# Optimization experiments

Hardware: AMD Instinct MI355X
Metric: run time of the kernel (lower is better)

Reference implementation:

```python
import jax, jax.numpy as jnp
import numpy as np

ALPHA, BETA, GAMMA = 1.0, 0.01, 0.1
COS_EPS = 1e-8  # torch F.cosine_similarity eps


def setup_inputs() -> dict:
    key = jax.random.key(0)
    k1, k2, k3, k4 = jax.random.split(key, 4)
    B, C = 4096, 1000
    N, D = 8192, 256
    return {
        "pred": jax.random.normal(k1, (B, C), dtype=jnp.float32),
        "target": jax.random.randint(k2, (B,), 0, C, dtype=jnp.int64),
        "adj_matrix": jax.random.uniform(k3, (N, N), dtype=jnp.float32),
        "node_embeddings": jax.random.normal(k4, (N, D), dtype=jnp.float32),
    }


def reference(pred, target, adj_matrix, node_embeddings):
    # L_task: mean cross-entropy over logits
    logp = jax.nn.log_softmax(pred, axis=-1)                      # [B, C]
    l_task = -jnp.mean(jnp.take_along_axis(logp, target[:, None], axis=1))

    # L_sparse: mean |adj|
    l_sparse = jnp.mean(jnp.abs(adj_matrix))

    # L_semantic: cosine similarity via normalize + matmul (avoids NxNxD intermediate)
    norms = jnp.linalg.norm(node_embeddings, axis=1)              # [N]
    dots = node_embeddings @ node_embeddings.T                    # [N, N]
    sim = dots / jnp.maximum(norms[:, None] * norms[None, :], COS_EPS)
    l_semantic = jnp.mean(adj_matrix * (1.0 - sim))

    return ALPHA * l_task + BETA * l_sparse + GAMMA * l_semantic
```

## Files before the change

### kernel.cpp

```cpp
#include <hip/hip_runtime.h>
#include <hip/hip_bf16.h>
#include <stdint.h>
#include <stddef.h>

#define N_NODES 8192
#define DIM     256
#define BATCH   4096
#define CLASSES 1000
#define ALPHA_C 1.0f
#define BETA_C  0.01f
#define GAMMA_C 0.1f

typedef __bf16 bf16_t;
typedef __bf16 bf16x8 __attribute__((ext_vector_type(8)));
typedef __bf16 bf16x4 __attribute__((ext_vector_type(4)));
typedef float  f32x4  __attribute__((ext_vector_type(4)));
typedef float  f32x16 __attribute__((ext_vector_type(16)));

__device__ __forceinline__ void async16(const void* g, void* l) {
  __builtin_amdgcn_global_load_lds(
      (const __attribute__((address_space(1))) uint32_t*)g,
      (__attribute__((address_space(3))) uint32_t*)l, 16, 0, 0);
}

__global__ __launch_bounds__(256) void prep_kernel(
    const float* __restrict__ emb, bf16_t* __restrict__ U) {
  const int row = blockIdx.x;
  const int t = threadIdx.x;
  const float v = emb[(size_t)row * DIM + t];
  float sq = v * v;
  for (int off = 32; off; off >>= 1) sq += __shfl_down(sq, off);
  __shared__ float red[4];
  if ((t & 63) == 0) red[t >> 6] = sq;
  __syncthreads();
  const float total = red[0] + red[1] + red[2] + red[3];
  U[(size_t)row * DIM + t] = (bf16_t)(v * rsqrtf(total));
}

__global__ __launch_bounds__(256) void transpose_kernel(
    const bf16_t* __restrict__ U, bf16_t* __restrict__ Ut) {
  __shared__ bf16_t tile[64][72];
  const int i0 = blockIdx.x * 64, d0 = blockIdx.y * 64;
  const int t = threadIdx.x;
  const int r = t >> 3, c8 = (t & 7) * 8;
#pragma unroll
  for (int it = 0; it < 2; ++it) {
    const int row = r + it * 32;
    *(bf16x8*)&tile[row][c8] =
        *(const bf16x8*)&U[(size_t)(i0 + row) * DIM + d0 + c8];
  }
  __syncthreads();
#pragma unroll
  for (int it = 0; it < 2; ++it) {
    const int d = r + it * 32;
    bf16x8 v;
#pragma unroll
    for (int j = 0; j < 8; ++j) v[j] = tile[c8 + j][d];
    *(bf16x8*)&Ut[(size_t)(d0 + d) * N_NODES + i0 + c8] = v;
  }
}

__global__ __launch_bounds__(256) void ce_kernel(
    const float* __restrict__ pred, const int* __restrict__ target,
    float* __restrict__ out) {
  const int row = blockIdx.x;
  const int t = threadIdx.x;
  const float* p = pred + (size_t)row * CLASSES;

  float v[4];
  for (int k = 0; k < 4; ++k) {
    const int c = t + k * 256;
    v[k] = (c < CLASSES) ? p[c] : -INFINITY;
  }

  float m = fmaxf(fmaxf(v[0], v[1]), fmaxf(v[2], v[3]));
  for (int off = 32; off; off >>= 1) m = fmaxf(m, __shfl_down(m, off));

  __shared__ float red[8];
  const int wave = t >> 6, lane = t & 63;
  if (lane == 0) red[wave] = m;
  __syncthreads();
  if (t == 0) red[4] = fmaxf(fmaxf(red[0], red[1]), fmaxf(red[2], red[3]));
  __syncthreads();
  const float mx = red[4];

  float s = 0.f;
  for (int k = 0; k < 4; ++k) s += __expf(v[k] - mx);
  for (int off = 32; off; off >>= 1) s += __shfl_down(s, off);
  if (lane == 0) red[wave] = s;
  __syncthreads();
  if (t == 0) {
    float ssum = red[0] + red[1] + red[2] + red[3];
    float lse = mx + __logf(ssum);
    float loss = lse - p[target[row]];
    atomicAdd(out, loss * (ALPHA_C / (float)BATCH));
  }
}

#define BN 128
#define BK 64
#define KC 8
#define KW (N_NODES / KC)
#define NCHUNK (KW / BK)

__global__ __launch_bounds__(512, 2) void semantic_kernel(
    const float* __restrict__ adj, const bf16_t* __restrict__ U,
    const bf16_t* __restrict__ Ut, float* __restrict__ out) {
  __shared__ __align__(16) bf16_t lds_ut[2][DIM * BK];
  __shared__ __align__(16) float  lds_a[2][BN * BK];
  __shared__ float red[8];

  const int t = threadIdx.x;
  const int w = t >> 6, lane = t & 63;
  const int wm = w >> 2, wn = w & 3;
  const int m = lane & 31, h = lane >> 5;
  const int i0 = blockIdx.x * BN;
  const int k0 = blockIdx.y * KW;

  f32x16 acc[4] = {};
  float s_abs = 0.f, s_sum = 0.f;

  const int ut_rl = lane >> 3;
  const int ut_c = (lane & 7) ^ ut_rl;
  const int a_rl = lane >> 4;

  auto STAGE = [&](int buf, int ck) {
    const int ko = k0 + ck * BK;
#pragma unroll
    for (int ii = 0; ii < 4; ++ii) {
      const int rbase = ii * 64 + w * 8;
      async16(Ut + (size_t)(rbase + ut_rl) * N_NODES + ko + ut_c * 8,
              &lds_ut[buf][rbase * BK]);
    }
#pragma unroll
    for (int ii = 0; ii < 4; ++ii) {
      const int rbase = w * 16 + ii * 4;
      const int r = rbase + a_rl;
      const int c = (lane & 15) ^ (r & 15);
      async16(adj + (size_t)(i0 + r) * N_NODES + ko + c * 4,
              &lds_a[buf][rbase * BK]);
    }
  };

  STAGE(0, 0);
  __syncthreads();

  int buf = 0;
  for (int ck = 0; ck < NCHUNK; ++ck) {
    if (ck + 1 < NCHUNK) STAGE(buf ^ 1, ck + 1);
#pragma unroll
    for (int kk = 0; kk < 4; ++kk) {
      bf16x8 af[4];
#pragma unroll
      for (int mr = 0; mr < 4; ++mr) {
        const int rd = wm * 128 + mr * 32 + m;
        af[mr] = *(const bf16x8*)
            &lds_ut[buf][rd * BK + (((kk * 2 + h) ^ (rd & 7)) * 8)];
      }
      const int ri = wn * 32 + m;
      const int c0 = kk * 4 + h * 2;
      const f32x4 b0 =
          *(const f32x4*)&lds_a[buf][ri * BK + ((c0 ^ (ri & 15)) * 4)];
      const f32x4 b1 =
          *(const f32x4*)&lds_a[buf][ri * BK + (((c0 + 1) ^ (ri & 15)) * 4)];
      if (wm == 0) {
        s_abs += fabsf(b0[0]) + fabsf(b0[1]) + fabsf(b0[2]) + fabsf(b0[3]) +
                 fabsf(b1[0]) + fabsf(b1[1]) + fabsf(b1[2]) + fabsf(b1[3]);
        s_sum += b0[0] + b0[1] + b0[2] + b0[3] + b1[0] + b1[1] + b1[2] + b1[3];
      }
      bf16x8 bb;
      bb[0] = (bf16_t)b0[0]; bb[1] = (bf16_t)b0[1];
      bb[2] = (bf16_t)b0[2]; bb[3] = (bf16_t)b0[3];
      bb[4] = (bf16_t)b1[0]; bb[5] = (bf16_t)b1[1];
      bb[6] = (bf16_t)b1[2]; bb[7] = (bf16_t)b1[3];
#pragma unroll
      for (int mr = 0; mr < 4; ++mr)
        acc[mr] = __builtin_amdgcn_mfma_f32_32x32x16_bf16(af[mr], bb, acc[mr],
                                                          0, 0, 0);
    }
    __syncthreads();
    buf ^= 1;
  }

  float tr = 0.f;
  const bf16_t* Urow = U + (size_t)(i0 + wn * 32 + m) * DIM;
#pragma unroll
  for (int mr = 0; mr < 4; ++mr) {
#pragma unroll
    for (int rq = 0; rq < 4; ++rq) {
      const int d = wm * 128 + mr * 32 + rq * 8 + h * 4;
      const bf16x4 uu = *(const bf16x4*)&Urow[d];
      tr += acc[mr][rq * 4 + 0] * (float)uu[0] +
            acc[mr][rq * 4 + 1] * (float)uu[1] +
            acc[mr][rq * 4 + 2] * (float)uu[2] +
            acc[mr][rq * 4 + 3] * (float)uu[3];
    }
  }

  float contrib = -GAMMA_C * tr;
  if (wm == 0) contrib += BETA_C * s_abs + GAMMA_C * s_sum;
  for (int off = 32; off; off >>= 1) contrib += __shfl_down(contrib, off);
  if (lane == 0) red[w] = contrib;
  __syncthreads();
  if (t == 0) {
    float tot = 0.f;
    for (int i = 0; i < 8; ++i) tot += red[i];
    const float inv = 1.f / ((float)N_NODES * (float)N_NODES);
    atomicAdd(out, tot * inv);
  }
}

extern "C" void kernel_launch(void* const* d_in, const int* in_sizes, int n_in,
                              void* d_out, int out_size, void* d_ws,
                              size_t ws_size, hipStream_t stream) {
  const float* pred   = (const float*)d_in[0];
  const int*   target = (const int*)d_in[1];
  const float* adj    = (const float*)d_in[2];
  const float* emb    = (const float*)d_in[3];
  float* out = (float*)d_out;

  bf16_t* U  = (bf16_t*)d_ws;
  bf16_t* Ut = U + (size_t)N_NODES * DIM;

  hipMemsetAsync(d_out, 0, sizeof(float), stream);
  prep_kernel<<<N_NODES, 256, 0, stream>>>(emb, U);
  transpose_kernel<<<dim3(N_NODES / 64, DIM / 64), 256, 0, stream>>>(U, Ut);
  ce_kernel<<<BATCH, 256, 0, stream>>>(pred, target, out);
  semantic_kernel<<<dim3(N_NODES / BN, KC), 512, 0, stream>>>(adj, U, Ut, out);
}
```

Measured before the change: 508.0 us.

## Load adj directly into registers with prefetch; stage full Ut slice once

The semantic kernel no longer double-buffers both adj and Ut tiles through LDS with a barrier every chunk. Each block now works on a 256-wide K slice (32 K-splits instead of 8). The whole Ut slice for that slice is loaded into LDS once with an XOR swizzle and a single barrier. Adjacency values are read straight from global memory into registers, with an 8-deep software prefetch ring feeding the MFMA B operand. This removes the per-chunk LDS traffic and barriers for adj, but each wave must now read adj itself, with 8 wavefronts sharing rows only through cache. It also quadruples the number of blocks and atomics, uses 128KB of LDS per block, which may cut occupancy, and increases register pressure.

```diff
diff --git a/kernel.cpp b/kernel.cpp
--- a/kernel.cpp
+++ b/kernel.cpp
@@ -98,16 +98,15 @@
 }
 
 #define BN 128
-#define BK 64
-#define KC 8
-#define KW (N_NODES / KC)
-#define NCHUNK (KW / BK)
+#define KW 256
+#define KC (N_NODES / KW)
+#define NKS (KW / 16)
+#define PF 8
 
 __global__ __launch_bounds__(512, 2) void semantic_kernel(
     const float* __restrict__ adj, const bf16_t* __restrict__ U,
     const bf16_t* __restrict__ Ut, float* __restrict__ out) {
-  __shared__ __align__(16) bf16_t lds_ut[2][DIM * BK];
-  __shared__ __align__(16) float  lds_a[2][BN * BK];
+  __shared__ __align__(16) bf16_t lds_ut[DIM * KW];
   __shared__ float red[8];
 
   const int t = threadIdx.x;
@@ -120,66 +119,60 @@
   f32x16 acc[4] = {};
   float s_abs = 0.f, s_sum = 0.f;
 
-  const int ut_rl = lane >> 3;
-  const int ut_c = (lane & 7) ^ ut_rl;
-  const int a_rl = lane >> 4;
-
-  auto STAGE = [&](int buf, int ck) {
-    const int ko = k0 + ck * BK;
-#pragma unroll
-    for (int ii = 0; ii < 4; ++ii) {
-      const int rbase = ii * 64 + w * 8;
-      async16(Ut + (size_t)(rbase + ut_rl) * N_NODES + ko + ut_c * 8,
-              &lds_ut[buf][rbase * BK]);
-    }
-#pragma unroll
-    for (int ii = 0; ii < 4; ++ii) {
-      const int rbase = w * 16 + ii * 4;
-      const int r = rbase + a_rl;
-      const int c = (lane & 15) ^ (r & 15);
-      async16(adj + (size_t)(i0 + r) * N_NODES + ko + c * 4,
-              &lds_a[buf][rbase * BK]);
-    }
-  };
-
-  STAGE(0, 0);
-  __syncthreads();
-
-  int buf = 0;
-  for (int ck = 0; ck < NCHUNK; ++ck) {
-    if (ck + 1 < NCHUNK) STAGE(buf ^ 1, ck + 1);
-#pragma unroll
-    for (int kk = 0; kk < 4; ++kk) {
-      bf16x8 af[4];
-#pragma unroll
-      for (int mr = 0; mr < 4; ++mr) {
-        const int rd = wm * 128 + mr * 32 + m;
-        af[mr] = *(const bf16x8*)
-            &lds_ut[buf][rd * BK + (((kk * 2 + h) ^ (rd & 7)) * 8)];
-      }
-      const int ri = wn * 32 + m;
-      const int c0 = kk * 4 + h * 2;
-      const f32x4 b0 =
-          *(const f32x4*)&lds_a[buf][ri * BK + ((c0 ^ (ri & 15)) * 4)];
-      const f32x4 b1 =
-          *(const f32x4*)&lds_a[buf][ri * BK + (((c0 + 1) ^ (ri & 15)) * 4)];
-      if (wm == 0) {
-        s_abs += fabsf(b0[0]) + fabsf(b0[1]) + fabsf(b0[2]) + fabsf(b0[3]) +
-                 fabsf(b1[0]) + fabsf(b1[1]) + fabsf(b1[2]) + fabsf(b1[3]);
-        s_sum += b0[0] + b0[1] + b0[2] + b0[3] + b1[0] + b1[1] + b1[2] + b1[3];
-      }
-      bf16x8 bb;
-      bb[0] = (bf16_t)b0[0]; bb[1] = (bf16_t)b0[1];
-      bb[2] = (bf16_t)b0[2]; bb[3] = (bf16_t)b0[3];
-      bb[4] = (bf16_t)b1[0]; bb[5] = (bf16_t)b1[1];
-      bb[6] = (bf16_t)b1[2]; bb[7] = (bf16_t)b1[3];
-#pragma unroll
-      for (int mr = 0; mr < 4; ++mr)
-        acc[mr] = __builtin_amdgcn_mfma_f32_32x32x16_bf16(af[mr], bb, acc[mr],
-                                                          0, 0, 0);
-    }
-    __syncthreads();
-    buf ^= 1;
+  const float* ap = adj + (size_t)(i0 + wn * 32 + m) * N_NODES + k0 + h * 8;
+
+  f32x4 pb[PF][2];
+#pragma unroll
+  for (int ks = 0; ks < PF; ++ks) {
+    pb[ks][0] = *(const f32x4*)(ap + ks * 16);
+    pb[ks][1] = *(const f32x4*)(ap + ks * 16 + 4);
+  }
+
+  {
+    const int rl = lane >> 5;
+    const int p = lane & 31;
+#pragma unroll
+    for (int ii = 0; ii < 16; ++ii) {
+      const int rbase = w * 32 + ii * 2;
+      const int r = rbase + rl;
+      async16(Ut + (size_t)r * N_NODES + k0 + ((p ^ (r & 31)) * 8),
+              &lds_ut[rbase * KW]);
+    }
+  }
+  __syncthreads();
+
+#pragma unroll
+  for (int ks = 0; ks < NKS; ++ks) {
+    const int s = ks & (PF - 1);
+    const f32x4 b0 = pb[s][0];
+    const f32x4 b1 = pb[s][1];
+    if (ks + PF < NKS) {
+      pb[s][0] = *(const f32x4*)(ap + (ks + PF) * 16);
+      pb[s][1] = *(const f32x4*)(ap + (ks + PF) * 16 + 4);
+    }
+
+    bf16x8 af[4];
+#pragma unroll
+    for (int mr = 0; mr < 4; ++mr) {
+      const int rd = wm * 128 + mr * 32 + m;
+      af[mr] = *(const bf16x8*)&lds_ut[rd * KW + (((ks * 2 + h) ^ m) * 8)];
+    }
+
+    if (wm == 0) {
+      s_abs += fabsf(b0[0]) + fabsf(b0[1]) + fabsf(b0[2]) + fabsf(b0[3]) +
+               fabsf(b1[0]) + fabsf(b1[1]) + fabsf(b1[2]) + fabsf(b1[3]);
+      s_sum += b0[0] + b0[1] + b0[2] + b0[3] + b1[0] + b1[1] + b1[2] + b1[3];
+    }
+
+    bf16x8 bb;
+    bb[0] = (bf16_t)b0[0]; bb[1] = (bf16_t)b0[1];
+    bb[2] = (bf16_t)b0[2]; bb[3] = (bf16_t)b0[3];
+    bb[4] = (bf16_t)b1[0]; bb[5] = (bf16_t)b1[1];
+    bb[6] = (bf16_t)b1[2]; bb[7] = (bf16_t)b1[3];
+#pragma unroll
+    for (int mr = 0; mr < 4; ++mr)
+      acc[mr] = __builtin_amdgcn_mfma_f32_32x32x16_bf16(af[mr], bb, acc[mr],
+                                                        0, 0, 0);
   }
 
   float tr = 0.f;
```

New measurement: 485.3 us. 4.5% less time.
